# Kernel optimization log

Measured on AMD Instinct MI355X. Metric: run time of the kernel, lower is better.

Reference implementation:

```python
import jax, jax.numpy as jnp
import numpy as np

B, T, E, H = 2, 2048, 768, 12
DH = E // H  # per-head attention dim
EPS = 1e-5


def setup_inputs() -> dict:
    key = jax.random.key(0)
    ks = jax.random.split(key, 12)
    s = 0.02
    return {
        "x": jax.random.normal(ks[0], (B, T, E), dtype=jnp.float32),
        # stacked per-head projection weights: [H, E, DH], biases [H, DH]
        "Wq": jax.random.normal(ks[1], (H, E, DH), dtype=jnp.float32) * s,
        "bq": jax.random.normal(ks[2], (H, DH), dtype=jnp.float32) * s,
        "Wk": jax.random.normal(ks[3], (H, E, DH), dtype=jnp.float32) * s,
        "bk": jax.random.normal(ks[4], (H, DH), dtype=jnp.float32) * s,
        "Wv": jax.random.normal(ks[5], (H, E, DH), dtype=jnp.float32) * s,
        "bv": jax.random.normal(ks[6], (H, DH), dtype=jnp.float32) * s,
        "Wo": jax.random.normal(ks[7], (E, E), dtype=jnp.float32) * s,
        "bo": jax.random.normal(ks[8], (E,), dtype=jnp.float32) * s,
        "gamma": jnp.ones((E,), dtype=jnp.float32),
        "beta": jnp.zeros((E,), dtype=jnp.float32),
    }


def reference(x, Wq, bq, Wk, bk, Wv, bv, Wo, bo, gamma, beta):
    # per-head projections (heads stacked on axis h)
    q = jnp.einsum("bte,hed->bhtd", x, Wq) + bq[None, :, None, :]
    k = jnp.einsum("bte,hed->bhtd", x, Wk) + bk[None, :, None, :]
    v = jnp.einsum("bte,hed->bhtd", x, Wv) + bv[None, :, None, :]

    scores = jnp.einsum("bhtd,bhsd->bhts", q, k) / jnp.sqrt(jnp.float32(DH))
    causal = jnp.tril(jnp.ones((T, T), dtype=bool))  # True = keep
    scores = jnp.where(causal[None, None], scores, -jnp.inf)
    attn = jax.nn.softmax(scores, axis=-1)
    o = jnp.einsum("bhts,bhsd->bhtd", attn, v)  # [B,H,T,DH]

    # concat heads in head order -> [B,T,E]
    concat = jnp.transpose(o, (0, 2, 1, 3)).reshape(B, T, E)
    proj = concat @ Wo + bo

    # LayerNorm(proj) then residual add
    mu = jnp.mean(proj, axis=-1, keepdims=True)
    var = jnp.mean((proj - mu) ** 2, axis=-1, keepdims=True)
    normed = (proj - mu) * jax.lax.rsqrt(var + EPS) * gamma + beta
    return x + normed
```

## Files before the change

### kernel.cpp

```cpp
#include <hip/hip_runtime.h>
#include <stdint.h>

#define NROWS 4096
#define EMB   768
#define NQKV  2304
#define TSEQ  2048
#define VTSTR 2080
#define XSTR  800
#define WSTR  800
#define PSTR  800
#define NHEAD 12
#define NBH   24

typedef unsigned short u16;
typedef u16  ushort4v __attribute__((ext_vector_type(4)));
typedef u16  ushort8 __attribute__((ext_vector_type(8)));
typedef __bf16 bf16x8 __attribute__((ext_vector_type(8)));
typedef float f32x4 __attribute__((ext_vector_type(4)));

typedef const __attribute__((address_space(1))) void* gas_ptr;
typedef __attribute__((address_space(3))) void* las_ptr;

__device__ __forceinline__ u16 f2bf(float f) {
  union { float f; uint32_t u; } v; v.f = f;
  uint32_t u = v.u;
  return (u16)((u + 0x7fffu + ((u >> 16) & 1u)) >> 16);
}
__device__ __forceinline__ float bf2f(u16 u) {
  union { uint32_t u; float f; } v; v.u = ((uint32_t)u) << 16;
  return v.f;
}
__device__ __forceinline__ uint32_t cvtpk(float lo, float hi) {
  uint32_t r;
  asm("v_cvt_pk_bf16_f32 %0, %1, %2" : "=v"(r) : "v"(lo), "v"(hi));
  return r;
}

#define VMCNT0 asm volatile("s_waitcnt vmcnt(0)" ::: "memory")
#define LGKM0  asm volatile("s_waitcnt lgkmcnt(0)" ::: "memory")
#define SBAR   __builtin_amdgcn_s_barrier()
#define SCHED0 __builtin_amdgcn_sched_barrier(0)
#define MFMA(a, b, c) __builtin_amdgcn_mfma_f32_16x16x32_bf16((a), (b), (c), 0, 0, 0)

__global__ __launch_bounds__(256) void k_pack(const float* __restrict__ x, u16* __restrict__ xb,
                                              const float* __restrict__ Wq, const float* __restrict__ Wk,
                                              const float* __restrict__ Wv, u16* __restrict__ wt,
                                              const float* __restrict__ Wo, u16* __restrict__ wot,
                                              uint32_t* __restrict__ cnt, uint32_t* __restrict__ tbl) {
  int bid = blockIdx.x, tid = threadIdx.x;
  if (bid == 0) {
    if (tid < 8) cnt[tid] = 0;
    if (tid >= 64 && tid < 84) {
      int p = tid - 64;
      int myqi = 0, myc = 0, k = 0;
      for (int qi = 0; qi < 8; ++qi) {
        int nt = 4 * qi + 4;
        int nch = (nt + 7) >> 3;
        for (int c = 0; c < nch; ++c) { if (k == p) { myqi = qi; myc = c; } ++k; }
      }
      int nt = 4 * myqi + 4;
      int t0 = myc * 8;
      int t1 = (nt < t0 + 8) ? nt : t0 + 8;
      int mylen = t1 - t0, myid = myqi * 4 + myc;
      int rank = 0;
      for (int qi = 0; qi < 8; ++qi) {
        int nt2 = 4 * qi + 4;
        int nch = (nt2 + 7) >> 3;
        for (int c = 0; c < nch; ++c) {
          int u0 = c * 8;
          int u1 = (nt2 < u0 + 8) ? nt2 : u0 + 8;
          int l = u1 - u0, id = qi * 4 + c;
          if (l > mylen || (l == mylen && id < myid)) ++rank;
        }
      }
      tbl[rank] = (uint32_t)myqi | ((uint32_t)t0 << 8) | ((uint32_t)t1 << 16)
                | ((uint32_t)myc << 24) | (myqi <= 1 ? 0x80000000u : 0u);
    }
  }
  if (bid < 1536) {
    int i = bid * 2048 + tid * 8;
    int row = i / EMB, col = i - row * EMB;
    float4 a = *(const float4*)(x + i);
    float4 b = *(const float4*)(x + i + 4);
    uint4 o;
    o.x = cvtpk(a.x, a.y); o.y = cvtpk(a.z, a.w);
    o.z = cvtpk(b.x, b.y); o.w = cvtpk(b.z, b.w);
    *(uint4*)(xb + (size_t)row * XSTR + col) = o;
    return;
  }
  __shared__ u16 lds[64][68];
  if (bid < 1968) {
    int t = bid - 1536;
    int sel = t / 144, rest = t - sel * 144;
    int h = rest / 12, ec = rest - h * 12;
    const float* W = sel == 0 ? Wq : (sel == 1 ? Wk : Wv);
    const float* src = W + ((size_t)(h * EMB + ec * 64) * 64);
    int e = tid >> 2, d0 = (tid & 3) * 16;
#pragma unroll
    for (int j = 0; j < 4; ++j) {
      float4 v = *(const float4*)(src + (size_t)e * 64 + d0 + 4 * j);
      ushort4v pk;
      uint32_t w0 = cvtpk(v.x, v.y), w1 = cvtpk(v.z, v.w);
      pk[0] = (u16)(w0 & 0xffff); pk[1] = (u16)(w0 >> 16);
      pk[2] = (u16)(w1 & 0xffff); pk[3] = (u16)(w1 >> 16);
      *(ushort4v*)(&lds[e][d0 + 4 * j]) = pk;
    }
    __syncthreads();
    int d = tid >> 2, e0 = (tid & 3) * 16;
    ushort8 o0, o1;
#pragma unroll
    for (int j = 0; j < 8; ++j) { o0[j] = lds[e0 + j][d]; o1[j] = lds[e0 + 8 + j][d]; }
    int n = sel * EMB + h * 64 + d;
    u16* dst = wt + (size_t)n * WSTR + ec * 64 + e0;
    *(ushort8*)dst = o0;
    *(ushort8*)(dst + 8) = o1;
  } else {
    int t = bid - 1968;
    int er = t / 12, nc = t - er * 12;
    int e = tid >> 2, n0 = (tid & 3) * 16;
#pragma unroll
    for (int j = 0; j < 4; ++j) {
      float4 v = *(const float4*)(Wo + (size_t)(er * 64 + e) * EMB + nc * 64 + n0 + 4 * j);
      ushort4v pk;
      uint32_t w0 = cvtpk(v.x, v.y), w1 = cvtpk(v.z, v.w);
      pk[0] = (u16)(w0 & 0xffff); pk[1] = (u16)(w0 >> 16);
      pk[2] = (u16)(w1 & 0xffff); pk[3] = (u16)(w1 >> 16);
      *(ushort4v*)(&lds[e][n0 + 4 * j]) = pk;
    }
    __syncthreads();
    int n = tid >> 2, e0 = (tid & 3) * 16;
    ushort8 o0, o1;
#pragma unroll
    for (int j = 0; j < 8; ++j) { o0[j] = lds[e0 + j][n]; o1[j] = lds[e0 + 8 + j][n]; }
    u16* dst = wot + (size_t)(nc * 64 + n) * WSTR + er * 64 + e0;
    *(ushort8*)dst = o0;
    *(ushort8*)(dst + 8) = o1;
  }
}

template<int BM, int BN, int OUT_MODE>
__global__ __launch_bounds__(256) void k_gemm(const u16* __restrict__ A, const u16* __restrict__ Bt,
                                              const float* __restrict__ b0, const float* __restrict__ b1,
                                              const float* __restrict__ b2, void* __restrict__ Cout,
                                              u16* __restrict__ qpk, u16* __restrict__ kpk,
                                              u16* __restrict__ vtout,
                                              int M, int N, int K, int lda, int ldb) {
  constexpr int MR = BM / 32, NR = BN / 32;
  __shared__ u16 lds_a[BM * 64];
  __shared__ u16 lds_b[BN * 64];
  int tid = threadIdx.x;
  int w = tid >> 6, lane = tid & 63;
  int wr = w >> 1, wc = w & 1;
  int m0 = blockIdx.x * BM, n0 = blockIdx.y * BN;
  int lrow = lane & 15, g = lane >> 4;

  f32x4 zero = {0.f, 0.f, 0.f, 0.f};
  f32x4 acc[MR][NR];
  for (int m = 0; m < MR; ++m) for (int n = 0; n < NR; ++n) acc[m][n] = zero;

  int l8 = lane >> 3, c8 = lane & 7;

  for (int k0 = 0; k0 < K; k0 += 64) {
#pragma unroll
    for (int i = 0; i < BM / 32; ++i) {
      int row = w * (BM / 4) + 8 * i + l8;
      int c16 = c8 ^ (row & 7);
      const u16* ga = A + (size_t)(m0 + row) * lda + k0 + c16 * 8;
      __builtin_amdgcn_global_load_lds((gas_ptr)ga, (las_ptr)(lds_a + (w * (BM / 4) + 8 * i) * 64), 16, 0, 0);
    }
#pragma unroll
    for (int i = 0; i < BN / 32; ++i) {
      int row = w * (BN / 4) + 8 * i + l8;
      int c16 = c8 ^ (row & 7);
      const u16* gb = Bt + (size_t)(n0 + row) * ldb + k0 + c16 * 8;
      __builtin_amdgcn_global_load_lds((gas_ptr)gb, (las_ptr)(lds_b + (w * (BN / 4) + 8 * i) * 64), 16, 0, 0);
    }
    __syncthreads();
    bf16x8 af[MR][2], bfr[NR][2];
#pragma unroll
    for (int m = 0; m < MR; ++m)
#pragma unroll
      for (int kc = 0; kc < 2; ++kc) {
        int row = wr * (BM / 2) + m * 16 + lrow;
        int ch = (kc * 4 + g) ^ (row & 7);
        af[m][kc] = *(const bf16x8*)(lds_a + row * 64 + ch * 8);
      }
#pragma unroll
    for (int n = 0; n < NR; ++n)
#pragma unroll
      for (int kc = 0; kc < 2; ++kc) {
        int row = wc * (BN / 2) + n * 16 + lrow;
        int ch = (kc * 4 + g) ^ (row & 7);
        bfr[n][kc] = *(const bf16x8*)(lds_b + row * 64 + ch * 8);
      }
#pragma unroll
    for (int kc = 0; kc < 2; ++kc)
#pragma unroll
      for (int m = 0; m < MR; ++m)
#pragma unroll
        for (int n = 0; n < NR; ++n)
          acc[m][n] = MFMA(af[m][kc], bfr[n][kc], acc[m][n]);
    __syncthreads();
  }

#pragma unroll
  for (int m = 0; m < MR; ++m)
#pragma unroll
    for (int n = 0; n < NR; ++n) {
      int col = n0 + wc * (BN / 2) + n * 16 + lrow;
      float bcol;
      if (OUT_MODE == 1) bcol = b0[col];
      else {
        int sel = col >= 1536 ? 2 : (col >= 768 ? 1 : 0);
        const float* bs = sel == 0 ? b0 : (sel == 1 ? b1 : b2);
        bcol = bs[col - sel * EMB];
      }
      int row0 = m0 + wr * (BM / 2) + m * 16 + 4 * g;
      if (OUT_MODE == 2) {
        int sel = col >= 1536 ? 2 : (col >= 768 ? 1 : 0);
        int c = col - sel * EMB;
        int hh = c >> 6, d = c & 63;
        int bb = row0 >> 11, t = row0 & 2047;
        int y = bb * NHEAD + hh;
        if (sel == 2) {
          ushort4v pk;
#pragma unroll
          for (int r = 0; r < 4; ++r) pk[r] = f2bf(acc[m][n][r] + bcol);
          *(ushort4v*)(vtout + (size_t)(y * 64 + d) * VTSTR + t) = pk;
        } else {
          u16* dst = (sel == 0 ? qpk : kpk) + (size_t)(y * TSEQ + t) * 64 + d;
#pragma unroll
          for (int r = 0; r < 4; ++r) dst[r * 64] = f2bf(acc[m][n][r] + bcol);
        }
      } else {
#pragma unroll
        for (int r = 0; r < 4; ++r) {
          int row = row0 + r;
          ((float*)Cout)[(size_t)row * PSTR + col] = acc[m][n][r] + bcol;
        }
      }
    }
}

#define QKROW(SB) do { \
    bf16x8 ka0 = *(const bf16x8*)(kb + ((((SB) * 16 + ql) * 64 + 8 * g) ^ swz)); \
    bf16x8 ka1 = *(const bf16x8*)(kb + ((((SB) * 16 + ql) * 64 + 32 + 8 * g) ^ swz)); \
    st##SB##q0 = MFMA(ka0, bq00, st##SB##q0); st##SB##q0 = MFMA(ka1, bq01, st##SB##q0); \
    st##SB##q1 = MFMA(ka0, bq10, st##SB##q1); st##SB##q1 = MFMA(ka1, bq11, st##SB##q1); \
  } while (0)

#define SMX1(STV, SB, QC, LR) do { \
    float _v0 = __builtin_fmaf(STV[0], sc2, -2.0f); \
    float _v1 = __builtin_fmaf(STV[1], sc2, -2.0f); \
    float _v2 = __builtin_fmaf(STV[2], sc2, -2.0f); \
    float _v3 = __builtin_fmaf(STV[3], sc2, -2.0f); \
    if (maskt) { \
      int _sg = s0 + (SB) * 16 + 4 * g; \
      int _qq = qw0 + (QC) * 16 + ql; \
      if (_sg + 0 > _qq) _v0 = -1e30f; \
      if (_sg + 1 > _qq) _v1 = -1e30f; \
      if (_sg + 2 > _qq) _v2 = -1e30f; \
      if (_sg + 3 > _qq) _v3 = -1e30f; \
    } \
    float _e0 = __builtin_amdgcn_exp2f(_v0), _e1 = __builtin_amdgcn_exp2f(_v1); \
    float _e2 = __builtin_amdgcn_exp2f(_v2), _e3 = __builtin_amdgcn_exp2f(_v3); \
    LR += (_e0 + _e1) + (_e2 + _e3); \
    uint2 _dw; _dw.x = cvtpk(_e0, _e1); _dw.y = cvtpk(_e2, _e3); \
    *(uint2*)(pw + ((((QC) * 16 + ql) * 64 + (SB) * 16 + 4 * g) ^ swz)) = _dw; \
  } while (0)

#define PVROW(DB) do { \
    bf16x8 vb0 = *(const bf16x8*)(vb + ((((DB) * 16 + ql) * 64 + 8 * g) ^ swz)); \
    bf16x8 vb1 = *(const bf16x8*)(vb + ((((DB) * 16 + ql) * 64 + 32 + 8 * g) ^ swz)); \
    o##DB##q0 = MFMA(ap00, vb0, o##DB##q0); o##DB##q0 = MFMA(ap01, vb1, o##DB##q0); \
    o##DB##q1 = MFMA(ap10, vb0, o##DB##q1); o##DB##q1 = MFMA(ap11, vb1, o##DB##q1); \
  } while (0)

#define OUTD(DB, QC, PTR, STRIDE, L0, L1, L2, L3) do { \
    (PTR)[0 * (STRIDE) + (DB) * 16] = f2bf(o##DB##q##QC[0] * (L0)); \
    (PTR)[1 * (STRIDE) + (DB) * 16] = f2bf(o##DB##q##QC[1] * (L1)); \
    (PTR)[2 * (STRIDE) + (DB) * 16] = f2bf(o##DB##q##QC[2] * (L2)); \
    (PTR)[3 * (STRIDE) + (DB) * 16] = f2bf(o##DB##q##QC[3] * (L3)); \
  } while (0)

__global__ __launch_bounds__(512, 2) void k_attn(const u16* __restrict__ qpk, const u16* __restrict__ kpk,
                                                 const u16* __restrict__ vt,
                                                 u16* __restrict__ aout, uint32_t* __restrict__ cnt,
                                                 const uint32_t* __restrict__ tbl,
                                                 u16* __restrict__ pO, float* __restrict__ pL) {
  __shared__ u16 kbuf[2][64 * 64];
  __shared__ u16 vbuf[2][64 * 64];
  __shared__ u16 pbuf[8][32 * 64];
  int tid = threadIdx.x;
  int w = tid >> 6, lane = tid & 63;
  int ql = lane & 15, g = lane >> 4;
  int xcd = blockIdx.x & 7;
  const float sc2 = 0.18033688f;
  u16* pw = &pbuf[w][0];
  int swz = (ql & 7) << 3;
  int srow = tid >> 3, sc8 = tid & 7;
  volatile int* taskp = (volatile int*)&pbuf[0][0];
  f32x4 zero = {0.f, 0.f, 0.f, 0.f};

  for (;;) {
    if (tid == 0) *taskp = (int)atomicAdd(&cnt[xcd], 1u);
    __syncthreads();
    int tau = *taskp;
    __syncthreads();
    if (tau >= 60) break;

    int rank = tau / 3, yl = tau - rank * 3;
    uint32_t te = tbl[rank];
    int qi = te & 0xff, t0 = (te >> 8) & 0xff, t1ex = (te >> 16) & 0xff, cslot = (te >> 24) & 0x7f;
    bool direct = (te >> 31) != 0;

    int y = xcd * 3 + yl;
    int b = y / NHEAD, h = y - b * NHEAD;
    int qb0 = qi * 256, qw0 = qb0 + w * 32;
    int qtw = qw0 >> 6;

    const u16* qp0 = qpk + (size_t)(y * TSEQ + qw0 + ql) * 64;
    const u16* qp1 = qpk + (size_t)(y * TSEQ + qw0 + 16 + ql) * 64;
    bf16x8 bq00 = *(const bf16x8*)(qp0 + 8 * g);
    bf16x8 bq01 = *(const bf16x8*)(qp0 + 32 + 8 * g);
    bf16x8 bq10 = *(const bf16x8*)(qp1 + 8 * g);
    bf16x8 bq11 = *(const bf16x8*)(qp1 + 32 + 8 * g);

    const u16* kst = kpk + (size_t)y * TSEQ * 64;
    const u16* vst = vt + (size_t)y * 64 * VTSTR;

    f32x4 o0q0 = zero, o1q0 = zero, o2q0 = zero, o3q0 = zero;
    f32x4 o0q1 = zero, o1q1 = zero, o2q1 = zero, o3q1 = zero;
    float lr0 = 0.f, lr1 = 0.f;

    auto STAGE = [&](int bi, int t_) {
      int c16 = sc8 ^ (srow & 7);
      const u16* gk = kst + (size_t)t_ * 4096 + srow * 64 + c16 * 8;
      __builtin_amdgcn_global_load_lds((gas_ptr)gk, (las_ptr)(&kbuf[bi][(8 * w) * 64]), 16, 0, 0);
      const u16* gv = vst + (size_t)srow * VTSTR + t_ * 64 + c16 * 8;
      __builtin_amdgcn_global_load_lds((gas_ptr)gv, (las_ptr)(&vbuf[bi][(8 * w) * 64]), 16, 0, 0);
    };

    STAGE(t0 & 1, t0);
    for (int t = t0; t < t1ex; ++t) {
      int cur = t & 1;
      VMCNT0;
      SBAR;
      if (t + 1 < t1ex) STAGE(cur ^ 1, t + 1);

      const u16* kb = &kbuf[cur][0];
      const u16* vb = &vbuf[cur][0];
      int s0 = t * 64;
      bool maskt = (t >= qtw);

      f32x4 st0q0 = zero, st1q0 = zero, st2q0 = zero, st3q0 = zero;
      f32x4 st0q1 = zero, st1q1 = zero, st2q1 = zero, st3q1 = zero;
      QKROW(0); QKROW(1); QKROW(2); QKROW(3);

      SMX1(st0q0, 0, 0, lr0); SMX1(st1q0, 1, 0, lr0); SMX1(st2q0, 2, 0, lr0); SMX1(st3q0, 3, 0, lr0);
      SMX1(st0q1, 0, 1, lr1); SMX1(st1q1, 1, 1, lr1); SMX1(st2q1, 2, 1, lr1); SMX1(st3q1, 3, 1, lr1);

      LGKM0; SCHED0;
      bf16x8 ap00 = *(const bf16x8*)(pw + (((0 * 16 + ql) * 64 + 8 * g) ^ swz));
      bf16x8 ap01 = *(const bf16x8*)(pw + (((0 * 16 + ql) * 64 + 32 + 8 * g) ^ swz));
      bf16x8 ap10 = *(const bf16x8*)(pw + (((1 * 16 + ql) * 64 + 8 * g) ^ swz));
      bf16x8 ap11 = *(const bf16x8*)(pw + (((1 * 16 + ql) * 64 + 32 + 8 * g) ^ swz));

      PVROW(0); PVROW(1); PVROW(2); PVROW(3);
    }

    float lw0 = lr0, lw1 = lr1;
    lw0 += __shfl_xor(lw0, 16); lw0 += __shfl_xor(lw0, 32);
    lw1 += __shfl_xor(lw1, 16); lw1 += __shfl_xor(lw1, 32);

    if (direct) {
      float li0 = 1.0f / lw0, li1 = 1.0f / lw1;
      float a0 = __shfl(li0, 4 * g + 0), a1 = __shfl(li0, 4 * g + 1);
      float a2 = __shfl(li0, 4 * g + 2), a3 = __shfl(li0, 4 * g + 3);
      u16* ab0 = aout + (size_t)(b * TSEQ + qw0 + 4 * g) * XSTR + h * 64 + ql;
      OUTD(0, 0, ab0, XSTR, a0, a1, a2, a3); OUTD(1, 0, ab0, XSTR, a0, a1, a2, a3);
      OUTD(2, 0, ab0, XSTR, a0, a1, a2, a3); OUTD(3, 0, ab0, XSTR, a0, a1, a2, a3);
      float c0 = __shfl(li1, 4 * g + 0), c1 = __shfl(li1, 4 * g + 1);
      float c2 = __shfl(li1, 4 * g + 2), c3 = __shfl(li1, 4 * g + 3);
      u16* ab1 = aout + (size_t)(b * TSEQ + qw0 + 16 + 4 * g) * XSTR + h * 64 + ql;
      OUTD(0, 1, ab1, XSTR, c0, c1, c2, c3); OUTD(1, 1, ab1, XSTR, c0, c1, c2, c3);
      OUTD(2, 1, ab1, XSTR, c0, c1, c2, c3); OUTD(3, 1, ab1, XSTR, c0, c1, c2, c3);
    } else {
      int blk2 = (y * 8 + qi) * 4 + cslot;
      u16* po = pO + (size_t)blk2 * 16384;
      float* pl = pL + (size_t)blk2 * 256;
      if (g == 0) { pl[w * 32 + ql] = lw0; pl[w * 32 + 16 + ql] = lw1; }
      u16* pb0 = po + (w * 32 + 4 * g) * 64 + ql;
      OUTD(0, 0, pb0, 64, 1.f, 1.f, 1.f, 1.f); OUTD(1, 0, pb0, 64, 1.f, 1.f, 1.f, 1.f);
      OUTD(2, 0, pb0, 64, 1.f, 1.f, 1.f, 1.f); OUTD(3, 0, pb0, 64, 1.f, 1.f, 1.f, 1.f);
      u16* pb1 = po + (w * 32 + 16 + 4 * g) * 64 + ql;
      OUTD(0, 1, pb1, 64, 1.f, 1.f, 1.f, 1.f); OUTD(1, 1, pb1, 64, 1.f, 1.f, 1.f, 1.f);
      OUTD(2, 1, pb1, 64, 1.f, 1.f, 1.f, 1.f); OUTD(3, 1, pb1, 64, 1.f, 1.f, 1.f, 1.f);
    }
  }
}

__global__ __launch_bounds__(256) void k_combine(const u16* __restrict__ pO, const float* __restrict__ pL,
                                                 u16* __restrict__ aout) {
  int blk = blockIdx.x;
  int u = blk >> 2, quarter = blk & 3;
  int y = u >> 3, qi = u & 7;
  int nch = (4 * qi + 4 + 7) >> 3;
  if (nch < 2) return;
  int b = y / NHEAD, h = y - b * NHEAD;
  int tid = threadIdx.x;
  int rl = quarter * 64 + (tid >> 2), c0 = (tid & 3) * 16;
  float l = 0.f;
#pragma unroll 4
  for (int c = 0; c < 4; ++c)
    if (c < nch) l += pL[((size_t)u * 4 + c) * 256 + rl];
  float rinv = 1.0f / l;
  float acc[16];
#pragma unroll
  for (int j = 0; j < 16; ++j) acc[j] = 0.f;
#pragma unroll 4
  for (int c = 0; c < 4; ++c)
    if (c < nch) {
      const u16* p = pO + ((size_t)u * 4 + c) * 16384 + rl * 64 + c0;
      ushort8 a0 = *(const ushort8*)p;
      ushort8 a1 = *(const ushort8*)(p + 8);
#pragma unroll
      for (int j = 0; j < 8; ++j) { acc[j] += bf2f(a0[j]); acc[8 + j] += bf2f(a1[j]); }
    }
  ushort8 o0, o1;
#pragma unroll
  for (int j = 0; j < 8; j += 2) {
    uint32_t w0 = cvtpk(acc[j] * rinv, acc[j + 1] * rinv);
    o0[j] = (u16)(w0 & 0xffff); o0[j + 1] = (u16)(w0 >> 16);
    uint32_t w1 = cvtpk(acc[8 + j] * rinv, acc[9 + j] * rinv);
    o1[j] = (u16)(w1 & 0xffff); o1[j + 1] = (u16)(w1 >> 16);
  }
  u16* dst = aout + (size_t)(b * TSEQ + qi * 256 + rl) * XSTR + h * 64 + c0;
  *(ushort8*)dst = o0;
  *(ushort8*)(dst + 8) = o1;
}

__global__ __launch_bounds__(256) void k_ln_res(const float* __restrict__ proj, const float* __restrict__ x,
                                                const float* __restrict__ gamma, const float* __restrict__ beta,
                                                float* __restrict__ out) {
  __shared__ float smem[2][4];
  int row = blockIdx.x;
  const float* pr = proj + (size_t)row * PSTR;
  const float* xr = x + (size_t)row * EMB;
  float* orow = out + (size_t)row * EMB;
  int tid = threadIdx.x;
  float v[3];
  float s = 0.f, s2 = 0.f;
#pragma unroll
  for (int i = 0; i < 3; ++i) { v[i] = pr[tid + 256 * i]; s += v[i]; s2 += v[i] * v[i]; }
#pragma unroll
  for (int m = 1; m < 64; m <<= 1) { s += __shfl_xor(s, m); s2 += __shfl_xor(s2, m); }
  int w = tid >> 6, lane = tid & 63;
  if (lane == 0) { smem[0][w] = s; smem[1][w] = s2; }
  __syncthreads();
  s  = smem[0][0] + smem[0][1] + smem[0][2] + smem[0][3];
  s2 = smem[1][0] + smem[1][1] + smem[1][2] + smem[1][3];
  float mu = s * (1.f / EMB);
  float var = s2 * (1.f / EMB) - mu * mu;
  float rstd = rsqrtf(var + 1e-5f);
#pragma unroll
  for (int i = 0; i < 3; ++i) {
    int c = tid + 256 * i;
    orow[c] = xr[c] + (v[i] - mu) * rstd * gamma[c] + beta[c];
  }
}

extern "C" void kernel_launch(void* const* d_in, const int* in_sizes, int n_in,
                              void* d_out, int out_size, void* d_ws, size_t ws_size,
                              hipStream_t stream) {
  const float* x     = (const float*)d_in[0];
  const float* Wq    = (const float*)d_in[1];
  const float* bq    = (const float*)d_in[2];
  const float* Wk    = (const float*)d_in[3];
  const float* bk    = (const float*)d_in[4];
  const float* Wv    = (const float*)d_in[5];
  const float* bv    = (const float*)d_in[6];
  const float* Wo    = (const float*)d_in[7];
  const float* bo    = (const float*)d_in[8];
  const float* gamma = (const float*)d_in[9];
  const float* beta  = (const float*)d_in[10];
  float* out = (float*)d_out;

  char* ws = (char*)d_ws;
  size_t off = 0;
  u16* xb    = (u16*)(ws + off); off += (size_t)NROWS * XSTR * 2;
  u16* wqkvt = (u16*)(ws + off); off += (size_t)NQKV * WSTR * 2;
  u16* wot   = (u16*)(ws + off); off += (size_t)EMB * WSTR * 2;
  uint32_t* cnt = (uint32_t*)(ws + off); off += 64;
  uint32_t* tbl = (uint32_t*)(ws + off); off += 512;
  u16* qpk   = (u16*)(ws + off); off += (size_t)NBH * TSEQ * 64 * 2;
  u16* kpk   = (u16*)(ws + off); off += (size_t)NBH * TSEQ * 64 * 2;
  u16* vt    = (u16*)(ws + off); off += (size_t)NBH * 64 * VTSTR * 2;
  u16* aout  = (u16*)(ws + off); off += (size_t)NROWS * XSTR * 2;
  u16* pO    = (u16*)(ws + off); off += (size_t)NBH * 8 * 4 * 16384 * 2;
  float* pL  = (float*)(ws + off); off += (size_t)NBH * 8 * 4 * 256 * 4;
  float* proj = (float*)qpk;

  k_pack<<<dim3(2112), 256, 0, stream>>>(x, xb, Wq, Wk, Wv, wqkvt, Wo, wot, cnt, tbl);
  k_gemm<128, 128, 2><<<dim3(NROWS / 128, NQKV / 128), 256, 0, stream>>>(
      xb, wqkvt, bq, bk, bv, nullptr, qpk, kpk, vt, NROWS, NQKV, EMB, XSTR, WSTR);
  k_attn<<<dim3(512), 512, 0, stream>>>(qpk, kpk, vt, aout, cnt, tbl, pO, pL);
  k_combine<<<dim3(768), 256, 0, stream>>>(pO, pL, aout);
  k_gemm<128, 64, 1><<<dim3(NROWS / 128, EMB / 64), 256, 0, stream>>>(
      aout, wot, bo, nullptr, nullptr, proj, nullptr, nullptr, nullptr, NROWS, EMB, EMB, XSTR, WSTR);
  k_ln_res<<<NROWS, 256, 0, stream>>>(proj, x, gamma, beta, out);
}
```

Measured before the change: 118.1 us.

## Rebalance attention split-KV chunks, add MFMA priority, bf16 projection, warp-per-row LayerNorm

```diff
diff --git a/kernel.cpp b/kernel.cpp
--- a/kernel.cpp
+++ b/kernel.cpp
@@ -50,31 +50,28 @@
   int bid = blockIdx.x, tid = threadIdx.x;
   if (bid == 0) {
     if (tid < 8) cnt[tid] = 0;
-    if (tid >= 64 && tid < 84) {
+    if (tid >= 64 && tid < 90) {
       int p = tid - 64;
       int myqi = 0, myc = 0, k = 0;
       for (int qi = 0; qi < 8; ++qi) {
-        int nt = 4 * qi + 4;
-        int nch = (nt + 7) >> 3;
+        int nch = (qi + 1 < 4) ? qi + 1 : 4;
         for (int c = 0; c < nch; ++c) { if (k == p) { myqi = qi; myc = c; } ++k; }
       }
-      int nt = 4 * myqi + 4;
-      int t0 = myc * 8;
-      int t1 = (nt < t0 + 8) ? nt : t0 + 8;
-      int mylen = t1 - t0, myid = myqi * 4 + myc;
+      int mynch = (myqi + 1 < 4) ? myqi + 1 : 4;
+      int mylen = (4 * myqi + 4) / mynch;
+      int t0 = myc * mylen, t1 = t0 + mylen;
+      int myid = myqi * 4 + myc;
       int rank = 0;
       for (int qi = 0; qi < 8; ++qi) {
-        int nt2 = 4 * qi + 4;
-        int nch = (nt2 + 7) >> 3;
+        int nch = (qi + 1 < 4) ? qi + 1 : 4;
+        int len = (4 * qi + 4) / nch;
         for (int c = 0; c < nch; ++c) {
-          int u0 = c * 8;
-          int u1 = (nt2 < u0 + 8) ? nt2 : u0 + 8;
-          int l = u1 - u0, id = qi * 4 + c;
-          if (l > mylen || (l == mylen && id < myid)) ++rank;
+          int id = qi * 4 + c;
+          if (len > mylen || (len == mylen && id < myid)) ++rank;
         }
       }
       tbl[rank] = (uint32_t)myqi | ((uint32_t)t0 << 8) | ((uint32_t)t1 << 16)
-                | ((uint32_t)myc << 24) | (myqi <= 1 ? 0x80000000u : 0u);
+                | ((uint32_t)myc << 24) | (myqi == 0 ? 0x80000000u : 0u);
     }
   }
   if (bid < 1536) {
@@ -236,7 +233,7 @@
 #pragma unroll
         for (int r = 0; r < 4; ++r) {
           int row = row0 + r;
-          ((float*)Cout)[(size_t)row * PSTR + col] = acc[m][n][r] + bcol;
+          ((u16*)Cout)[(size_t)row * PSTR + col] = f2bf(acc[m][n][r] + bcol);
         }
       }
     }
@@ -307,7 +304,7 @@
     __syncthreads();
     int tau = *taskp;
     __syncthreads();
-    if (tau >= 60) break;
+    if (tau >= 78) break;
 
     int rank = tau / 3, yl = tau - rank * 3;
     uint32_t te = tbl[rank];
@@ -355,7 +352,9 @@
 
       f32x4 st0q0 = zero, st1q0 = zero, st2q0 = zero, st3q0 = zero;
       f32x4 st0q1 = zero, st1q1 = zero, st2q1 = zero, st3q1 = zero;
+      __builtin_amdgcn_s_setprio(1);
       QKROW(0); QKROW(1); QKROW(2); QKROW(3);
+      __builtin_amdgcn_s_setprio(0);
 
       SMX1(st0q0, 0, 0, lr0); SMX1(st1q0, 1, 0, lr0); SMX1(st2q0, 2, 0, lr0); SMX1(st3q0, 3, 0, lr0);
       SMX1(st0q1, 0, 1, lr1); SMX1(st1q1, 1, 1, lr1); SMX1(st2q1, 2, 1, lr1); SMX1(st3q1, 3, 1, lr1);
@@ -366,7 +365,9 @@
       bf16x8 ap10 = *(const bf16x8*)(pw + (((1 * 16 + ql) * 64 + 8 * g) ^ swz));
       bf16x8 ap11 = *(const bf16x8*)(pw + (((1 * 16 + ql) * 64 + 32 + 8 * g) ^ swz));
 
+      __builtin_amdgcn_s_setprio(1);
       PVROW(0); PVROW(1); PVROW(2); PVROW(3);
+      __builtin_amdgcn_s_setprio(0);
     }
 
     float lw0 = lr0, lw1 = lr1;
@@ -405,7 +406,7 @@
   int blk = blockIdx.x;
   int u = blk >> 2, quarter = blk & 3;
   int y = u >> 3, qi = u & 7;
-  int nch = (4 * qi + 4 + 7) >> 3;
+  int nch = (qi + 1 < 4) ? qi + 1 : 4;
   if (nch < 2) return;
   int b = y / NHEAD, h = y - b * NHEAD;
   int tid = threadIdx.x;
@@ -440,34 +441,48 @@
   *(ushort8*)(dst + 8) = o1;
 }
 
-__global__ __launch_bounds__(256) void k_ln_res(const float* __restrict__ proj, const float* __restrict__ x,
+__global__ __launch_bounds__(256) void k_ln_res(const u16* __restrict__ proj, const float* __restrict__ x,
                                                 const float* __restrict__ gamma, const float* __restrict__ beta,
                                                 float* __restrict__ out) {
-  __shared__ float smem[2][4];
-  int row = blockIdx.x;
-  const float* pr = proj + (size_t)row * PSTR;
+  int w = threadIdx.x >> 6, lane = threadIdx.x & 63;
+  int row = blockIdx.x * 4 + w;
+  const u16* pr = proj + (size_t)row * PSTR;
   const float* xr = x + (size_t)row * EMB;
   float* orow = out + (size_t)row * EMB;
-  int tid = threadIdx.x;
-  float v[3];
+  int c0 = 12 * lane;
+  ushort4v p0 = *(const ushort4v*)(pr + c0);
+  ushort4v p1 = *(const ushort4v*)(pr + c0 + 4);
+  ushort4v p2 = *(const ushort4v*)(pr + c0 + 8);
+  float v[12];
+#pragma unroll
+  for (int j = 0; j < 4; ++j) { v[j] = bf2f(p0[j]); v[4 + j] = bf2f(p1[j]); v[8 + j] = bf2f(p2[j]); }
   float s = 0.f, s2 = 0.f;
 #pragma unroll
-  for (int i = 0; i < 3; ++i) { v[i] = pr[tid + 256 * i]; s += v[i]; s2 += v[i] * v[i]; }
+  for (int j = 0; j < 12; ++j) { s += v[j]; s2 += v[j] * v[j]; }
 #pragma unroll
   for (int m = 1; m < 64; m <<= 1) { s += __shfl_xor(s, m); s2 += __shfl_xor(s2, m); }
-  int w = tid >> 6, lane = tid & 63;
-  if (lane == 0) { smem[0][w] = s; smem[1][w] = s2; }
-  __syncthreads();
-  s  = smem[0][0] + smem[0][1] + smem[0][2] + smem[0][3];
-  s2 = smem[1][0] + smem[1][1] + smem[1][2] + smem[1][3];
   float mu = s * (1.f / EMB);
   float var = s2 * (1.f / EMB) - mu * mu;
   float rstd = rsqrtf(var + 1e-5f);
-#pragma unroll
-  for (int i = 0; i < 3; ++i) {
-    int c = tid + 256 * i;
-    orow[c] = xr[c] + (v[i] - mu) * rstd * gamma[c] + beta[c];
-  }
+  float4 xv0 = *(const float4*)(xr + c0);
+  float4 xv1 = *(const float4*)(xr + c0 + 4);
+  float4 xv2 = *(const float4*)(xr + c0 + 8);
+  float4 g0 = *(const float4*)(gamma + c0);
+  float4 g1 = *(const float4*)(gamma + c0 + 4);
+  float4 g2 = *(const float4*)(gamma + c0 + 8);
+  float4 b0 = *(const float4*)(beta + c0);
+  float4 b1 = *(const float4*)(beta + c0 + 4);
+  float4 b2 = *(const float4*)(beta + c0 + 8);
+  float4 o0, o1, o2;
+#pragma unroll
+  for (int j = 0; j < 4; ++j) {
+    o0[j] = xv0[j] + (v[j]     - mu) * rstd * g0[j] + b0[j];
+    o1[j] = xv1[j] + (v[4 + j] - mu) * rstd * g1[j] + b1[j];
+    o2[j] = xv2[j] + (v[8 + j] - mu) * rstd * g2[j] + b2[j];
+  }
+  *(float4*)(orow + c0) = o0;
+  *(float4*)(orow + c0 + 4) = o1;
+  *(float4*)(orow + c0 + 8) = o2;
 }
 
 extern "C" void kernel_launch(void* const* d_in, const int* in_sizes, int n_in,
@@ -499,7 +514,7 @@
   u16* aout  = (u16*)(ws + off); off += (size_t)NROWS * XSTR * 2;
   u16* pO    = (u16*)(ws + off); off += (size_t)NBH * 8 * 4 * 16384 * 2;
   float* pL  = (float*)(ws + off); off += (size_t)NBH * 8 * 4 * 256 * 4;
-  float* proj = (float*)qpk;
+  u16* proj = qpk;
 
   k_pack<<<dim3(2112), 256, 0, stream>>>(x, xb, Wq, Wk, Wv, wqkvt, Wo, wot, cnt, tbl);
   k_gemm<128, 128, 2><<<dim3(NROWS / 128, NQKV / 128), 256, 0, stream>>>(
@@ -508,5 +523,5 @@
   k_combine<<<dim3(768), 256, 0, stream>>>(pO, pL, aout);
   k_gemm<128, 64, 1><<<dim3(NROWS / 128, EMB / 64), 256, 0, stream>>>(
       aout, wot, bo, nullptr, nullptr, proj, nullptr, nullptr, nullptr, NROWS, EMB, EMB, XSTR, WSTR);
-  k_ln_res<<<NROWS, 256, 0, stream>>>(proj, x, gamma, beta, out);
-}
+  k_ln_res<<<NROWS / 4, 256, 0, stream>>>(proj, x, gamma, beta, out);
+}
```

Measured after the change: 120.9 us. 1.02x slower.
